# Performance work log

Hardware: AMD Instinct MI355X
Metric: run time of the kernel (lower is better)

The kernel has to match this reference:

```python
import jax, jax.numpy as jnp
import numpy as np

D_MODEL = 1024
N_HEADS = 16
D_K = D_MODEL // N_HEADS


def rotate_half(x):
    x1, x2 = x[..., : x.shape[-1] // 2], x[..., x.shape[-1] // 2:]
    return jnp.concatenate((-x2, x1), axis=-1)


def rope_cos_sin(seq_len, d_k, dtype):
    inv_freq = 1.0 / (10000.0 ** (jnp.arange(0, d_k, 2, dtype=jnp.float32) / d_k))
    t = jnp.arange(seq_len, dtype=jnp.float32)
    freqs = jnp.outer(t, inv_freq)            # [S, d_k/2]
    emb = jnp.concatenate((freqs, freqs), -1) # [S, d_k]
    return jnp.cos(emb).astype(dtype), jnp.sin(emb).astype(dtype)


def setup_inputs() -> dict:
    key = jax.random.key(0)
    ks = jax.random.split(key, 8)
    B, S = 1, 2048
    q = jax.random.normal(ks[0], (B, S, D_MODEL), jnp.float32)
    k = jax.random.normal(ks[1], (B, S, D_MODEL), jnp.float32)
    v = jax.random.normal(ks[2], (B, S, D_MODEL), jnp.float32)
    # xavier-uniform-ish weights for [d_model, d_model]
    bound = float(np.sqrt(6.0 / (D_MODEL + D_MODEL)))
    def W(kk):
        return jax.random.uniform(kk, (D_MODEL, D_MODEL), jnp.float32, -bound, bound)
    return {
        "query": q, "key": k, "value": v,
        "w_q": W(ks[3]), "w_k": W(ks[4]), "w_v": W(ks[5]),
        "w_o": W(ks[6]), "b_o": jnp.zeros((D_MODEL,), jnp.float32),
    }


def reference(query, key, value, w_q, w_k, w_v, w_o, b_o):
    B, Sq, _ = query.shape
    Sk = key.shape[1]
    # projections (torch Linear: x @ W.T)
    Q = (query @ w_q.T).reshape(B, Sq, N_HEADS, D_K).transpose(0, 2, 1, 3)
    K = (key @ w_k.T).reshape(B, Sk, N_HEADS, D_K).transpose(0, 2, 1, 3)
    V = (value @ w_v.T).reshape(B, Sk, N_HEADS, D_K).transpose(0, 2, 1, 3)
    # RoPE on Q and K (over head dim d_k)
    cos_q, sin_q = rope_cos_sin(Sq, D_K, Q.dtype)
    cos_k, sin_k = (cos_q, sin_q) if Sk == Sq else rope_cos_sin(Sk, D_K, K.dtype)
    Q = Q * cos_q + rotate_half(Q) * sin_q
    K = K * cos_k + rotate_half(K) * sin_k
    scores = jnp.einsum("bhqd,bhkd->bhqk", Q, K) / jnp.sqrt(jnp.float32(D_K)).astype(Q.dtype)
    attn = jax.nn.softmax(scores, axis=-1)          # [B,H,Sq,Sk]
    ctx = jnp.einsum("bhqk,bhkd->bhqd", attn, V)    # [B,H,Sq,d_k]
    ctx = ctx.transpose(0, 2, 1, 3).reshape(B, Sq, D_MODEL)
    out = ctx @ w_o.T + b_o
    return out, attn
```

## Files before the change

### kernel.cpp

```cpp
#include <hip/hip_runtime.h>
#include <hip/hip_bf16.h>

using short8 = __attribute__((ext_vector_type(8))) short;
using f32x4  = __attribute__((ext_vector_type(4))) float;

#define SEQ   2048
#define DM    1024
#define NHEAD 16
#define MB    1048576

static __device__ __forceinline__ short f2bf(float f) {
    union { __hip_bfloat16 b; short s; } u;
    u.b = __float2bfloat16(f);
    return u.s;
}
static __device__ __forceinline__ float bf2f(short s) {
    union { __hip_bfloat16 b; short s16; } u;
    u.s16 = s;
    return __bfloat162float(u.b);
}
static __device__ __forceinline__ f32x4 mfma_bf16(short8 a, short8 b, f32x4 c) {
    return __builtin_amdgcn_mfma_f32_16x16x32_bf16(a, b, c, 0, 0, 0);
}

__global__ __launch_bounds__(256) void prep_kernel(
    const float* __restrict__ q, const float* __restrict__ k, const float* __restrict__ v,
    const float* __restrict__ wq, const float* __restrict__ wk, const float* __restrict__ wv,
    const float* __restrict__ wo, short* __restrict__ bf,
    float* __restrict__ cosT, float* __restrict__ sinT)
{
    long t = (long)blockIdx.x * 256 + threadIdx.x;
    if (t < 1310720) {
        long e0 = t * 8;
        const float* src; long off;
        if      (e0 < 2L*MB) { src = q;  off = e0; }
        else if (e0 < 4L*MB) { src = k;  off = e0 - 2L*MB; }
        else if (e0 < 6L*MB) { src = v;  off = e0 - 4L*MB; }
        else if (e0 < 7L*MB) { src = wq; off = e0 - 6L*MB; }
        else if (e0 < 8L*MB) { src = wk; off = e0 - 7L*MB; }
        else if (e0 < 9L*MB) { src = wv; off = e0 - 8L*MB; }
        else                 { src = wo; off = e0 - 9L*MB; }
        float4 a = *(const float4*)(src + off);
        float4 b = *(const float4*)(src + off + 4);
        short8 o;
        o[0]=f2bf(a.x); o[1]=f2bf(a.y); o[2]=f2bf(a.z); o[3]=f2bf(a.w);
        o[4]=f2bf(b.x); o[5]=f2bf(b.y); o[6]=f2bf(b.z); o[7]=f2bf(b.w);
        *(short8*)(bf + e0) = o;
    } else {
        long tt = t - 1310720;
        int s = (int)(tt >> 5), j = (int)(tt & 31);
        float invf = __expf(-(float)j * (9.210340371976184f / 32.0f));
        float arg = (float)s * invf;
        cosT[tt] = cosf(arg);
        sinT[tt] = sinf(arg);
    }
}

__global__ __launch_bounds__(256, 2) void gemm_kernel(
    short* __restrict__ wsbf, const float* __restrict__ bo,
    float* __restrict__ out, int kind)
{
    __shared__ short As[128 * 64];
    __shared__ short Bs[128 * 64];
    const int tid  = threadIdx.x;
    const int lane = tid & 63;
    const int wave = tid >> 6;
    const int q4   = lane >> 4;
    const int l16  = lane & 15;
    const int wm   = wave >> 1;
    const int wn   = wave & 1;
    const int m0   = blockIdx.y * 128;
    const int n0   = blockIdx.x * 128;
    const int z    = blockIdx.z;

    const short* A; const short* W;
    if (kind == 0) { A = wsbf + (size_t)z * (2*MB); W = wsbf + 6*(size_t)MB + (size_t)z * MB; }
    else           { A = wsbf + 16*(size_t)MB;      W = wsbf + 9*(size_t)MB; }

    f32x4 zero = {0.f, 0.f, 0.f, 0.f};
    f32x4 acc[4][4];
    #pragma unroll
    for (int i = 0; i < 4; ++i)
        #pragma unroll
        for (int j = 0; j < 4; ++j) acc[i][j] = zero;

    for (int k0 = 0; k0 < 1024; k0 += 64) {
        __syncthreads();
        #pragma unroll
        for (int r = 0; r < 4; ++r) {
            int g = r * 256 + tid;
            int row = g >> 3, c8 = g & 7;
            int sw = c8 ^ (row & 7);
            *(short8*)&As[row*64 + sw*8] = *(const short8*)(A + (size_t)(m0+row)*1024 + k0 + c8*8);
            *(short8*)&Bs[row*64 + sw*8] = *(const short8*)(W + (size_t)(n0+row)*1024 + k0 + c8*8);
        }
        __syncthreads();
        #pragma unroll
        for (int kk = 0; kk < 2; ++kk) {
            short8 af[4], bfr[4];
            #pragma unroll
            for (int i = 0; i < 4; ++i) {
                int ra = wm*64 + i*16 + l16;
                af[i]  = *(const short8*)&As[ra*64 + (((kk*4+q4) ^ (ra&7))*8)];
                int rb = wn*64 + i*16 + l16;
                bfr[i] = *(const short8*)&Bs[rb*64 + (((kk*4+q4) ^ (rb&7))*8)];
            }
            #pragma unroll
            for (int i = 0; i < 4; ++i)
                #pragma unroll
                for (int j = 0; j < 4; ++j)
                    acc[i][j] = mfma_bf16(af[i], bfr[j], acc[i][j]);
        }
    }

    #pragma unroll
    for (int i = 0; i < 4; ++i) {
        #pragma unroll
        for (int j = 0; j < 4; ++j) {
            #pragma unroll
            for (int jj = 0; jj < 4; ++jj) {
                int gr = m0 + wm*64 + i*16 + q4*4 + jj;
                int gc = n0 + wn*64 + j*16 + l16;
                float val = acc[i][j][jj];
                if (kind == 0) {
                    int h = gc >> 6, d = gc & 63;
                    if (z < 2) {
                        short* dst = wsbf + (size_t)(10 + 2*z) * MB;
                        dst[((size_t)h*SEQ + gr)*64 + d] = f2bf(val);
                    } else {
                        short* dst = wsbf + (size_t)14 * MB;
                        dst[((size_t)h*64 + d)*SEQ + gr] = f2bf(val);
                    }
                } else {
                    out[(size_t)gr*1024 + gc] = val + bo[gc];
                }
            }
        }
    }
}

__global__ __launch_bounds__(256) void rope_kernel(
    short* __restrict__ Qh, short* __restrict__ Kh,
    const float* __restrict__ cosT, const float* __restrict__ sinT)
{
    int t = blockIdx.x * 256 + threadIdx.x;
    short* P = blockIdx.y ? Kh : Qh;
    int j = t & 31;
    int s = (t >> 5) & 2047;
    int h = t >> 16;
    size_t base = ((size_t)h * SEQ + s) * 64;
    float c  = cosT[(s << 5) + j];
    float sn = sinT[(s << 5) + j];
    float x1 = bf2f(P[base + j]);
    float x2 = bf2f(P[base + j + 32]);
    P[base + j]      = f2bf(x1 * c - x2 * sn);
    P[base + j + 32] = f2bf(x2 * c + x1 * sn);
}

__global__ __launch_bounds__(256, 2) void rowsum_kernel(
    const short* __restrict__ wsbf, float* __restrict__ rowsum)
{
    __shared__ short Qs[64 * 64];
    __shared__ short Ks[128 * 64];
    const int tid = threadIdx.x, lane = tid & 63, wave = tid >> 6;
    const int q4 = lane >> 4, l16 = lane & 15;
    const int h = blockIdx.y, qt0 = blockIdx.x * 64;
    const short* Qg = wsbf + (size_t)10*MB + ((size_t)h*SEQ + qt0)*64;
    const short* Kg = wsbf + (size_t)12*MB + (size_t)h*SEQ*64;
    #pragma unroll
    for (int r = 0; r < 2; ++r) {
        int g = r*256 + tid; int row = g >> 3, c8 = g & 7;
        *(short8*)&Qs[row*64 + ((c8 ^ (row&7))*8)] = *(const short8*)(Qg + (size_t)row*64 + c8*8);
    }
    float rs[4] = {0.f, 0.f, 0.f, 0.f};
    const int ra = wave*16 + l16;
    for (int kt = 0; kt < 16; ++kt) {
        __syncthreads();
        #pragma unroll
        for (int r = 0; r < 4; ++r) {
            int g = r*256 + tid; int row = g >> 3, c8 = g & 7;
            *(short8*)&Ks[row*64 + ((c8 ^ (row&7))*8)] =
                *(const short8*)(Kg + (size_t)(kt*128 + row)*64 + c8*8);
        }
        __syncthreads();
        #pragma unroll
        for (int nt = 0; nt < 8; ++nt) {
            f32x4 acc = {0.f, 0.f, 0.f, 0.f};
            #pragma unroll
            for (int kk = 0; kk < 2; ++kk) {
                short8 a = *(const short8*)&Qs[ra*64 + (((kk*4+q4) ^ (ra&7))*8)];
                int rb = nt*16 + l16;
                short8 b = *(const short8*)&Ks[rb*64 + (((kk*4+q4) ^ (rb&7))*8)];
                acc = mfma_bf16(a, b, acc);
            }
            #pragma unroll
            for (int jj = 0; jj < 4; ++jj) rs[jj] += __expf(acc[jj] * 0.125f);
        }
    }
    #pragma unroll
    for (int jj = 0; jj < 4; ++jj)
        #pragma unroll
        for (int m = 1; m < 16; m <<= 1)
            rs[jj] += __shfl_xor(rs[jj], m);
    if (l16 == 0) {
        float* rp = rowsum + h*SEQ + qt0 + wave*16 + q4*4;
        rp[0] = rs[0]; rp[1] = rs[1]; rp[2] = rs[2]; rp[3] = rs[3];
    }
}

__global__ __launch_bounds__(256, 2) void attn_kernel(
    const short* __restrict__ wsbf, short* __restrict__ ctxout,
    const float* __restrict__ rowsum, float* __restrict__ attn)
{
    __shared__ short Qs[64 * 64];
    __shared__ short Ks[128 * 64];
    __shared__ short Vs[64 * 128];
    __shared__ short Ps[4][16 * 128];
    const int tid = threadIdx.x, lane = tid & 63, wave = tid >> 6;
    const int q4 = lane >> 4, l16 = lane & 15;
    const int h = blockIdx.y, qt0 = blockIdx.x * 64;
    const short* Qg = wsbf + (size_t)10*MB + ((size_t)h*SEQ + qt0)*64;
    const short* Kg = wsbf + (size_t)12*MB + (size_t)h*SEQ*64;
    const short* Vg = wsbf + (size_t)14*MB + (size_t)h*64*SEQ;
    #pragma unroll
    for (int r = 0; r < 2; ++r) {
        int g = r*256 + tid; int row = g >> 3, c8 = g & 7;
        *(short8*)&Qs[row*64 + ((c8 ^ (row&7))*8)] = *(const short8*)(Qg + (size_t)row*64 + c8*8);
    }
    const int qbase = qt0 + wave*16 + q4*4;
    float irs[4];
    #pragma unroll
    for (int jj = 0; jj < 4; ++jj) irs[jj] = 1.0f / rowsum[h*SEQ + qbase + jj];
    f32x4 zero = {0.f, 0.f, 0.f, 0.f};
    f32x4 ctx[4] = {zero, zero, zero, zero};
    float* arow = attn + (size_t)h*SEQ*SEQ;
    const int ra = wave*16 + l16;

    for (int kt = 0; kt < 16; ++kt) {
        __syncthreads();
        #pragma unroll
        for (int r = 0; r < 4; ++r) {
            int g = r*256 + tid; int row = g >> 3, c8 = g & 7;
            *(short8*)&Ks[row*64 + ((c8 ^ (row&7))*8)] =
                *(const short8*)(Kg + (size_t)(kt*128 + row)*64 + c8*8);
        }
        #pragma unroll
        for (int r = 0; r < 4; ++r) {
            int g = r*256 + tid; int row = g >> 4, c16 = g & 15;
            *(short8*)&Vs[row*128 + ((c16 ^ (row&7))*8)] =
                *(const short8*)(Vg + (size_t)row*SEQ + kt*128 + c16*8);
        }
        __syncthreads();
        #pragma unroll
        for (int nt = 0; nt < 8; ++nt) {
            f32x4 acc = zero;
            #pragma unroll
            for (int kk = 0; kk < 2; ++kk) {
                short8 a = *(const short8*)&Qs[ra*64 + (((kk*4+q4) ^ (ra&7))*8)];
                int rb = nt*16 + l16;
                short8 b = *(const short8*)&Ks[rb*64 + (((kk*4+q4) ^ (rb&7))*8)];
                acc = mfma_bf16(a, b, acc);
            }
            #pragma unroll
            for (int jj = 0; jj < 4; ++jj) {
                float p = __expf(acc[jj] * 0.125f) * irs[jj];
                arow[(size_t)(qbase + jj)*SEQ + kt*128 + nt*16 + l16] = p;
                int prow = q4*4 + jj;
                int col  = nt*16 + l16;
                Ps[wave][prow*128 + (((col >> 3) ^ (prow & 7))*8) + (col & 7)] = f2bf(p);
            }
        }
        __syncthreads();
        #pragma unroll
        for (int kks = 0; kks < 4; ++kks) {
            short8 a = *(const short8*)&Ps[wave][l16*128 + (((kks*4+q4) ^ (l16 & 7))*8)];
            #pragma unroll
            for (int dt = 0; dt < 4; ++dt) {
                int rv = dt*16 + l16;
                short8 b = *(const short8*)&Vs[rv*128 + (((kks*4+q4) ^ (rv & 7))*8)];
                ctx[dt] = mfma_bf16(a, b, ctx[dt]);
            }
        }
    }
    #pragma unroll
    for (int dt = 0; dt < 4; ++dt)
        #pragma unroll
        for (int jj = 0; jj < 4; ++jj)
            ctxout[(size_t)(qbase + jj)*1024 + h*64 + dt*16 + l16] = f2bf(ctx[dt][jj]);
}

extern "C" void kernel_launch(void* const* d_in, const int* in_sizes, int n_in,
                              void* d_out, int out_size, void* d_ws, size_t ws_size,
                              hipStream_t stream)
{
    const float* q  = (const float*)d_in[0];
    const float* k  = (const float*)d_in[1];
    const float* v  = (const float*)d_in[2];
    const float* wq = (const float*)d_in[3];
    const float* wk = (const float*)d_in[4];
    const float* wv = (const float*)d_in[5];
    const float* wo = (const float*)d_in[6];
    const float* bo = (const float*)d_in[7];

    short* wsbf   = (short*)d_ws;
    float* fws    = (float*)((char*)d_ws + (size_t)36*MB);
    float* rowsum = fws;
    float* cosT   = fws + 32768;
    float* sinT   = cosT + 65536;
    float* out    = (float*)d_out;
    float* attn   = out + (size_t)SEQ*DM;

    hipLaunchKernelGGL(prep_kernel, dim3(5376), dim3(256), 0, stream,
                       q, k, v, wq, wk, wv, wo, wsbf, cosT, sinT);
    hipLaunchKernelGGL(gemm_kernel, dim3(8, 16, 3), dim3(256), 0, stream,
                       wsbf, bo, out, 0);
    hipLaunchKernelGGL(rope_kernel, dim3(4096, 2), dim3(256), 0, stream,
                       wsbf + (size_t)10*MB, wsbf + (size_t)12*MB, cosT, sinT);
    hipLaunchKernelGGL(rowsum_kernel, dim3(32, 16), dim3(256), 0, stream,
                       wsbf, rowsum);
    hipLaunchKernelGGL(attn_kernel, dim3(32, 16), dim3(256), 0, stream,
                       wsbf, wsbf + (size_t)16*MB, rowsum, attn);
    hipLaunchKernelGGL(gemm_kernel, dim3(8, 16, 1), dim3(256), 0, stream,
                       wsbf, bo, out, 1);
}
```

Baseline: 443.6 us.

## Fuse RoPE into QKV GEMM epilogue and merge rowsum into attention kernel

Applies RoPE directly in the QKV projection epilogue, so the separate rope kernel and its bf16 round trip go away. The standalone rowsum kernel is dropped: the attention kernel now accumulates unnormalized exp sums while computing P·V, normalizes ctx at the end, then runs a second QK pass to write normalized attention probabilities. It also hoists the Q fragments into registers, removes one barrier per tile, changes the P swizzle, and splits the output GEMM into 128x64 tiles for more blocks. QK^T is still computed twice, but two launches and a global rowsum buffer are removed.

```diff
diff --git a/kernel.cpp b/kernel.cpp
--- a/kernel.cpp
+++ b/kernel.cpp
@@ -13,11 +13,6 @@
     union { __hip_bfloat16 b; short s; } u;
     u.b = __float2bfloat16(f);
     return u.s;
-}
-static __device__ __forceinline__ float bf2f(short s) {
-    union { __hip_bfloat16 b; short s16; } u;
-    u.s16 = s;
-    return __bfloat162float(u.b);
 }
 static __device__ __forceinline__ f32x4 mfma_bf16(short8 a, short8 b, f32x4 c) {
     return __builtin_amdgcn_mfma_f32_16x16x32_bf16(a, b, c, 0, 0, 0);
@@ -56,9 +51,9 @@
     }
 }
 
-__global__ __launch_bounds__(256, 2) void gemm_kernel(
-    short* __restrict__ wsbf, const float* __restrict__ bo,
-    float* __restrict__ out, int kind)
+__global__ __launch_bounds__(256, 2) void gemm_qkv(
+    short* __restrict__ wsbf, const float* __restrict__ cosT,
+    const float* __restrict__ sinT)
 {
     __shared__ short As[128 * 64];
     __shared__ short Bs[128 * 64];
@@ -73,9 +68,8 @@
     const int n0   = blockIdx.x * 128;
     const int z    = blockIdx.z;
 
-    const short* A; const short* W;
-    if (kind == 0) { A = wsbf + (size_t)z * (2*MB); W = wsbf + 6*(size_t)MB + (size_t)z * MB; }
-    else           { A = wsbf + 16*(size_t)MB;      W = wsbf + 9*(size_t)MB; }
+    const short* A = wsbf + (size_t)z * (2*MB);
+    const short* W = wsbf + 6*(size_t)MB + (size_t)z * MB;
 
     f32x4 zero = {0.f, 0.f, 0.f, 0.f};
     f32x4 acc[4][4];
@@ -113,104 +107,43 @@
         }
     }
 
-    #pragma unroll
-    for (int i = 0; i < 4; ++i) {
-        #pragma unroll
-        for (int j = 0; j < 4; ++j) {
+    const int h = (n0 >> 6) + wn;
+    if (z < 2) {
+        short* dst = wsbf + (size_t)(10 + 2*z) * MB;
+        #pragma unroll
+        for (int i = 0; i < 4; ++i) {
             #pragma unroll
             for (int jj = 0; jj < 4; ++jj) {
-                int gr = m0 + wm*64 + i*16 + q4*4 + jj;
-                int gc = n0 + wn*64 + j*16 + l16;
-                float val = acc[i][j][jj];
-                if (kind == 0) {
-                    int h = gc >> 6, d = gc & 63;
-                    if (z < 2) {
-                        short* dst = wsbf + (size_t)(10 + 2*z) * MB;
-                        dst[((size_t)h*SEQ + gr)*64 + d] = f2bf(val);
-                    } else {
-                        short* dst = wsbf + (size_t)14 * MB;
-                        dst[((size_t)h*64 + d)*SEQ + gr] = f2bf(val);
-                    }
-                } else {
-                    out[(size_t)gr*1024 + gc] = val + bo[gc];
+                int s = m0 + wm*64 + i*16 + q4*4 + jj;
+                float c0 = cosT[(s<<5) + l16],      s0 = sinT[(s<<5) + l16];
+                float c1 = cosT[(s<<5) + 16 + l16], s1 = sinT[(s<<5) + 16 + l16];
+                float v0 = acc[i][0][jj], v1 = acc[i][1][jj];
+                float v2 = acc[i][2][jj], v3 = acc[i][3][jj];
+                size_t base = ((size_t)h*SEQ + s)*64;
+                dst[base + l16]      = f2bf(v0*c0 - v2*s0);
+                dst[base + 16 + l16] = f2bf(v1*c1 - v3*s1);
+                dst[base + 32 + l16] = f2bf(v2*c0 + v0*s0);
+                dst[base + 48 + l16] = f2bf(v3*c1 + v1*s1);
+            }
+        }
+    } else {
+        short* dst = wsbf + (size_t)14 * MB;
+        #pragma unroll
+        for (int i = 0; i < 4; ++i)
+            #pragma unroll
+            for (int j = 0; j < 4; ++j)
+                #pragma unroll
+                for (int jj = 0; jj < 4; ++jj) {
+                    int s = m0 + wm*64 + i*16 + q4*4 + jj;
+                    int d = j*16 + l16;
+                    dst[((size_t)h*64 + d)*SEQ + s] = f2bf(acc[i][j][jj]);
                 }
-            }
-        }
-    }
-}
-
-__global__ __launch_bounds__(256) void rope_kernel(
-    short* __restrict__ Qh, short* __restrict__ Kh,
-    const float* __restrict__ cosT, const float* __restrict__ sinT)
-{
-    int t = blockIdx.x * 256 + threadIdx.x;
-    short* P = blockIdx.y ? Kh : Qh;
-    int j = t & 31;
-    int s = (t >> 5) & 2047;
-    int h = t >> 16;
-    size_t base = ((size_t)h * SEQ + s) * 64;
-    float c  = cosT[(s << 5) + j];
-    float sn = sinT[(s << 5) + j];
-    float x1 = bf2f(P[base + j]);
-    float x2 = bf2f(P[base + j + 32]);
-    P[base + j]      = f2bf(x1 * c - x2 * sn);
-    P[base + j + 32] = f2bf(x2 * c + x1 * sn);
-}
-
-__global__ __launch_bounds__(256, 2) void rowsum_kernel(
-    const short* __restrict__ wsbf, float* __restrict__ rowsum)
-{
-    __shared__ short Qs[64 * 64];
-    __shared__ short Ks[128 * 64];
-    const int tid = threadIdx.x, lane = tid & 63, wave = tid >> 6;
-    const int q4 = lane >> 4, l16 = lane & 15;
-    const int h = blockIdx.y, qt0 = blockIdx.x * 64;
-    const short* Qg = wsbf + (size_t)10*MB + ((size_t)h*SEQ + qt0)*64;
-    const short* Kg = wsbf + (size_t)12*MB + (size_t)h*SEQ*64;
-    #pragma unroll
-    for (int r = 0; r < 2; ++r) {
-        int g = r*256 + tid; int row = g >> 3, c8 = g & 7;
-        *(short8*)&Qs[row*64 + ((c8 ^ (row&7))*8)] = *(const short8*)(Qg + (size_t)row*64 + c8*8);
-    }
-    float rs[4] = {0.f, 0.f, 0.f, 0.f};
-    const int ra = wave*16 + l16;
-    for (int kt = 0; kt < 16; ++kt) {
-        __syncthreads();
-        #pragma unroll
-        for (int r = 0; r < 4; ++r) {
-            int g = r*256 + tid; int row = g >> 3, c8 = g & 7;
-            *(short8*)&Ks[row*64 + ((c8 ^ (row&7))*8)] =
-                *(const short8*)(Kg + (size_t)(kt*128 + row)*64 + c8*8);
-        }
-        __syncthreads();
-        #pragma unroll
-        for (int nt = 0; nt < 8; ++nt) {
-            f32x4 acc = {0.f, 0.f, 0.f, 0.f};
-            #pragma unroll
-            for (int kk = 0; kk < 2; ++kk) {
-                short8 a = *(const short8*)&Qs[ra*64 + (((kk*4+q4) ^ (ra&7))*8)];
-                int rb = nt*16 + l16;
-                short8 b = *(const short8*)&Ks[rb*64 + (((kk*4+q4) ^ (rb&7))*8)];
-                acc = mfma_bf16(a, b, acc);
-            }
-            #pragma unroll
-            for (int jj = 0; jj < 4; ++jj) rs[jj] += __expf(acc[jj] * 0.125f);
-        }
-    }
-    #pragma unroll
-    for (int jj = 0; jj < 4; ++jj)
-        #pragma unroll
-        for (int m = 1; m < 16; m <<= 1)
-            rs[jj] += __shfl_xor(rs[jj], m);
-    if (l16 == 0) {
-        float* rp = rowsum + h*SEQ + qt0 + wave*16 + q4*4;
-        rp[0] = rs[0]; rp[1] = rs[1]; rp[2] = rs[2]; rp[3] = rs[3];
     }
 }
 
 __global__ __launch_bounds__(256, 2) void attn_kernel(
     const short* __restrict__ wsbf, short* __restrict__ ctxout,
-    const float* __restrict__ rowsum, float* __restrict__ attn)
+    float* __restrict__ attn)
 {
     __shared__ short Qs[64 * 64];
     __shared__ short Ks[128 * 64];
@@ -222,19 +155,23 @@
     const short* Qg = wsbf + (size_t)10*MB + ((size_t)h*SEQ + qt0)*64;
     const short* Kg = wsbf + (size_t)12*MB + (size_t)h*SEQ*64;
     const short* Vg = wsbf + (size_t)14*MB + (size_t)h*64*SEQ;
+
     #pragma unroll
     for (int r = 0; r < 2; ++r) {
         int g = r*256 + tid; int row = g >> 3, c8 = g & 7;
         *(short8*)&Qs[row*64 + ((c8 ^ (row&7))*8)] = *(const short8*)(Qg + (size_t)row*64 + c8*8);
     }
-    const int qbase = qt0 + wave*16 + q4*4;
-    float irs[4];
-    #pragma unroll
-    for (int jj = 0; jj < 4; ++jj) irs[jj] = 1.0f / rowsum[h*SEQ + qbase + jj];
+    __syncthreads();
+    const int ra = wave*16 + l16;
+    short8 a_q[2];
+    #pragma unroll
+    for (int kk = 0; kk < 2; ++kk)
+        a_q[kk] = *(const short8*)&Qs[ra*64 + (((kk*4+q4) ^ (ra&7))*8)];
+
     f32x4 zero = {0.f, 0.f, 0.f, 0.f};
     f32x4 ctx[4] = {zero, zero, zero, zero};
-    float* arow = attn + (size_t)h*SEQ*SEQ;
-    const int ra = wave*16 + l16;
+    float rs[4] = {0.f, 0.f, 0.f, 0.f};
+    const int frw = ((l16 & 7) + 2*(l16 >> 3)) & 7;
 
     for (int kt = 0; kt < 16; ++kt) {
         __syncthreads();
@@ -256,37 +193,143 @@
             f32x4 acc = zero;
             #pragma unroll
             for (int kk = 0; kk < 2; ++kk) {
-                short8 a = *(const short8*)&Qs[ra*64 + (((kk*4+q4) ^ (ra&7))*8)];
                 int rb = nt*16 + l16;
                 short8 b = *(const short8*)&Ks[rb*64 + (((kk*4+q4) ^ (rb&7))*8)];
-                acc = mfma_bf16(a, b, acc);
+                acc = mfma_bf16(a_q[kk], b, acc);
             }
             #pragma unroll
             for (int jj = 0; jj < 4; ++jj) {
-                float p = __expf(acc[jj] * 0.125f) * irs[jj];
-                arow[(size_t)(qbase + jj)*SEQ + kt*128 + nt*16 + l16] = p;
+                float p = __expf(acc[jj] * 0.125f);
+                rs[jj] += p;
                 int prow = q4*4 + jj;
                 int col  = nt*16 + l16;
-                Ps[wave][prow*128 + (((col >> 3) ^ (prow & 7))*8) + (col & 7)] = f2bf(p);
-            }
-        }
-        __syncthreads();
+                int fr   = ((prow & 7) + 2*(prow >> 3)) & 7;
+                int phys = (col >> 3) ^ fr;
+                Ps[wave][prow*128 + phys*8 + (col & 7)] = f2bf(p);
+            }
+        }
         #pragma unroll
         for (int kks = 0; kks < 4; ++kks) {
-            short8 a = *(const short8*)&Ps[wave][l16*128 + (((kks*4+q4) ^ (l16 & 7))*8)];
+            short8 a = *(const short8*)&Ps[wave][l16*128 + (((kks*4+q4) ^ frw)*8)];
             #pragma unroll
             for (int dt = 0; dt < 4; ++dt) {
                 int rv = dt*16 + l16;
-                short8 b = *(const short8*)&Vs[rv*128 + (((kks*4+q4) ^ (rv & 7))*8)];
+                short8 b = *(const short8*)&Vs[rv*128 + (((kks*4+q4) ^ (rv&7))*8)];
                 ctx[dt] = mfma_bf16(a, b, ctx[dt]);
             }
         }
     }
+
+    #pragma unroll
+    for (int jj = 0; jj < 4; ++jj)
+        #pragma unroll
+        for (int m = 1; m < 16; m <<= 1)
+            rs[jj] += __shfl_xor(rs[jj], m);
+    float irs[4];
+    #pragma unroll
+    for (int jj = 0; jj < 4; ++jj) irs[jj] = 1.0f / rs[jj];
+
+    const int qbase = qt0 + wave*16 + q4*4;
     #pragma unroll
     for (int dt = 0; dt < 4; ++dt)
         #pragma unroll
         for (int jj = 0; jj < 4; ++jj)
-            ctxout[(size_t)(qbase + jj)*1024 + h*64 + dt*16 + l16] = f2bf(ctx[dt][jj]);
+            ctxout[(size_t)(qbase + jj)*1024 + h*64 + dt*16 + l16] = f2bf(ctx[dt][jj] * irs[jj]);
+
+    float* arow = attn + (size_t)h*SEQ*SEQ;
+    for (int kt = 0; kt < 16; ++kt) {
+        __syncthreads();
+        #pragma unroll
+        for (int r = 0; r < 4; ++r) {
+            int g = r*256 + tid; int row = g >> 3, c8 = g & 7;
+            *(short8*)&Ks[row*64 + ((c8 ^ (row&7))*8)] =
+                *(const short8*)(Kg + (size_t)(kt*128 + row)*64 + c8*8);
+        }
+        __syncthreads();
+        #pragma unroll
+        for (int nt = 0; nt < 8; ++nt) {
+            f32x4 acc = zero;
+            #pragma unroll
+            for (int kk = 0; kk < 2; ++kk) {
+                int rb = nt*16 + l16;
+                short8 b = *(const short8*)&Ks[rb*64 + (((kk*4+q4) ^ (rb&7))*8)];
+                acc = mfma_bf16(a_q[kk], b, acc);
+            }
+            #pragma unroll
+            for (int jj = 0; jj < 4; ++jj)
+                arow[(size_t)(qbase + jj)*SEQ + kt*128 + nt*16 + l16] =
+                    __expf(acc[jj] * 0.125f) * irs[jj];
+        }
+    }
+}
+
+__global__ __launch_bounds__(256, 2) void gemm_out(
+    const short* __restrict__ wsbf, const float* __restrict__ bo,
+    float* __restrict__ out)
+{
+    __shared__ short As[128 * 64];
+    __shared__ short Bs[64 * 64];
+    const int tid = threadIdx.x, lane = tid & 63, wave = tid >> 6;
+    const int q4 = lane >> 4, l16 = lane & 15;
+    const int m0 = blockIdx.y * 128, n0 = blockIdx.x * 64;
+    const short* A = wsbf + 16*(size_t)MB;
+    const short* W = wsbf + 9*(size_t)MB;
+
+    f32x4 zero = {0.f, 0.f, 0.f, 0.f};
+    f32x4 acc[2][4];
+    #pragma unroll
+    for (int i = 0; i < 2; ++i)
+        #pragma unroll
+        for (int j = 0; j < 4; ++j) acc[i][j] = zero;
+
+    for (int k0 = 0; k0 < 1024; k0 += 64) {
+        __syncthreads();
+        #pragma unroll
+        for (int r = 0; r < 4; ++r) {
+            int g = r * 256 + tid;
+            int row = g >> 3, c8 = g & 7;
+            *(short8*)&As[row*64 + ((c8 ^ (row&7))*8)] =
+                *(const short8*)(A + (size_t)(m0+row)*1024 + k0 + c8*8);
+        }
+        #pragma unroll
+        for (int r = 0; r < 2; ++r) {
+            int g = r * 256 + tid;
+            int row = g >> 3, c8 = g & 7;
+            *(short8*)&Bs[row*64 + ((c8 ^ (row&7))*8)] =
+                *(const short8*)(W + (size_t)(n0+row)*1024 + k0 + c8*8);
+        }
+        __syncthreads();
+        #pragma unroll
+        for (int kk = 0; kk < 2; ++kk) {
+            short8 af[2], bfr[4];
+            #pragma unroll
+            for (int i = 0; i < 2; ++i) {
+                int ra = wave*32 + i*16 + l16;
+                af[i] = *(const short8*)&As[ra*64 + (((kk*4+q4) ^ (ra&7))*8)];
+            }
+            #pragma unroll
+            for (int j = 0; j < 4; ++j) {
+                int rb = j*16 + l16;
+                bfr[j] = *(const short8*)&Bs[rb*64 + (((kk*4+q4) ^ (rb&7))*8)];
+            }
+            #pragma unroll
+            for (int i = 0; i < 2; ++i)
+                #pragma unroll
+                for (int j = 0; j < 4; ++j)
+                    acc[i][j] = mfma_bf16(af[i], bfr[j], acc[i][j]);
+        }
+    }
+
+    #pragma unroll
+    for (int i = 0; i < 2; ++i)
+        #pragma unroll
+        for (int j = 0; j < 4; ++j)
+            #pragma unroll
+            for (int jj = 0; jj < 4; ++jj) {
+                int gr = m0 + wave*32 + i*16 + q4*4 + jj;
+                int gc = n0 + j*16 + l16;
+                out[(size_t)gr*1024 + gc] = acc[i][j][jj] + bo[gc];
+            }
 }
 
 extern "C" void kernel_launch(void* const* d_in, const int* in_sizes, int n_in,
@@ -302,24 +345,18 @@
     const float* wo = (const float*)d_in[6];
     const float* bo = (const float*)d_in[7];
 
-    short* wsbf   = (short*)d_ws;
-    float* fws    = (float*)((char*)d_ws + (size_t)36*MB);
-    float* rowsum = fws;
-    float* cosT   = fws + 32768;
-    float* sinT   = cosT + 65536;
-    float* out    = (float*)d_out;
-    float* attn   = out + (size_t)SEQ*DM;
+    short* wsbf = (short*)d_ws;
+    float* cosT = (float*)((char*)d_ws + (size_t)36*MB);
+    float* sinT = cosT + 65536;
+    float* out  = (float*)d_out;
+    float* attn = out + (size_t)SEQ*DM;
 
     hipLaunchKernelGGL(prep_kernel, dim3(5376), dim3(256), 0, stream,
                        q, k, v, wq, wk, wv, wo, wsbf, cosT, sinT);
-    hipLaunchKernelGGL(gemm_kernel, dim3(8, 16, 3), dim3(256), 0, stream,
-                       wsbf, bo, out, 0);
-    hipLaunchKernelGGL(rope_kernel, dim3(4096, 2), dim3(256), 0, stream,
-                       wsbf + (size_t)10*MB, wsbf + (size_t)12*MB, cosT, sinT);
-    hipLaunchKernelGGL(rowsum_kernel, dim3(32, 16), dim3(256), 0, stream,
-                       wsbf, rowsum);
+    hipLaunchKernelGGL(gemm_qkv, dim3(8, 16, 3), dim3(256), 0, stream,
+                       wsbf, cosT, sinT);
     hipLaunchKernelGGL(attn_kernel, dim3(32, 16), dim3(256), 0, stream,
-                       wsbf, wsbf + (size_t)16*MB, rowsum, attn);
-    hipLaunchKernelGGL(gemm_kernel, dim3(8, 16, 1), dim3(256), 0, stream,
-                       wsbf, bo, out, 1);
-}
+                       wsbf, wsbf + (size_t)16*MB, attn);
+    hipLaunchKernelGGL(gemm_out, dim3(16, 16), dim3(256), 0, stream,
+                       wsbf, bo, out);
+}
```

After: 402.2 us. -9.3%, faster.
